# Kernel optimization log

Measured on AMD Instinct MI355X. Metric: run time of the kernel, lower is better.

The kernel has to match this reference:

```python
import jax, jax.numpy as jnp
import numpy as np

# BERT-base dims; 768 and max_sent_num=64 come from the module/config.
N, S, V, D, L, H, F = 8, 512, 30522, 768, 12, 12, 3072
DH = D // H
MAX_SENT = 64
LN_EPS = 1e-12
SCALE = float(np.sqrt(DH))


def _ln(x, g, b):
    m = jnp.mean(x, axis=-1, keepdims=True)
    v = jnp.mean(jnp.square(x - m), axis=-1, keepdims=True)
    return (x - m) * jax.lax.rsqrt(v + LN_EPS) * g + b


def setup_inputs() -> dict:
    key = jax.random.key(0)
    ks = jax.random.split(key, 10)
    # random token ids in a range avoiding the special ids 102/103
    ids = jax.random.randint(ks[0], (N, S), 999, 30000, dtype=jnp.int32)
    # variable per-doc sentence region -> ragged number of [MASK](103) separators (8..64)
    cutoff = jax.random.randint(ks[1], (N, 1), 64, S + 1)
    pos = jnp.arange(S)[None, :]
    sent_pos = ((pos % 8) == 7) & (pos < cutoff)
    ids = jnp.where(sent_pos, 103, ids)
    ids = ids.at[:, 0].set(102)  # exactly one [SEP]=102 per doc (required by the slice-assign)
    amask = jnp.ones((N, S), dtype=jnp.int32)
    g = lambda k, shape: 0.02 * jax.random.normal(k, shape, dtype=jnp.float32)
    inp = dict(input_ids_bert=ids, attention_mask_bert=amask)
    inp["tok_emb"] = g(ks[2], (V, D))
    inp["pos_emb"] = g(ks[3], (S, D))
    inp["emb_ln_g"] = jnp.ones((D,), jnp.float32)
    inp["emb_ln_b"] = jnp.zeros((D,), jnp.float32)
    inp["Wqkv"] = g(ks[4], (L, D, 3 * D))
    inp["bqkv"] = jnp.zeros((L, 3 * D), jnp.float32)
    inp["Wo"] = g(ks[5], (L, D, D))
    inp["bo"] = jnp.zeros((L, D), jnp.float32)
    inp["ln1_g"] = jnp.ones((L, D), jnp.float32)
    inp["ln1_b"] = jnp.zeros((L, D), jnp.float32)
    inp["W1"] = g(ks[6], (L, D, F))
    inp["b1"] = jnp.zeros((L, F), jnp.float32)
    inp["W2"] = g(ks[7], (L, F, D))
    inp["b2"] = jnp.zeros((L, D), jnp.float32)
    inp["ln2_g"] = jnp.ones((L, D), jnp.float32)
    inp["ln2_b"] = jnp.zeros((L, D), jnp.float32)
    return inp


def _bert(ids, amask, tok_emb, pos_emb, emb_ln_g, emb_ln_b,
          Wqkv, bqkv, Wo, bo, ln1_g, ln1_b, W1, b1, W2, b2, ln2_g, ln2_b):
    x = tok_emb[ids] + pos_emb[None, :, :]            # [N,S,D]
    x = _ln(x, emb_ln_g, emb_ln_b)
    bias = (1.0 - amask[:, None, None, :].astype(x.dtype)) * -1e9  # [N,1,1,S]

    def layer(x, p):
        wqkv, bq, wo, bo_, g1, b1n, w1, b1f, w2, b2f, g2, b2n = p
        qkv = x @ wqkv + bq
        q, k, v = jnp.split(qkv, 3, axis=-1)
        q = q.reshape(N, S, H, DH)
        k = k.reshape(N, S, H, DH)
        v = v.reshape(N, S, H, DH)
        att = jnp.einsum('bqhd,bkhd->bhqk', q, k) / SCALE + bias
        att = jax.nn.softmax(att, axis=-1)
        o = jnp.einsum('bhqk,bkhd->bqhd', att, v).reshape(N, S, D)
        x2 = _ln(x + o @ wo + bo_, g1, b1n)
        h = jax.nn.gelu(x2 @ w1 + b1f, approximate=False)
        return _ln(x2 + h @ w2 + b2f, g2, b2n), None

    x, _ = jax.lax.scan(layer, x, (Wqkv, bqkv, Wo, bo, ln1_g, ln1_b, W1, b1, W2, b2, ln2_g, ln2_b))
    return x


def _gather_scatter(ids, h):
    # Vectorized form of the per-doc python loop:
    #   out[doc, :n_sent] = concat([cls_emb(102), sent_embs(103)])[:-1]
    mask_sent = ids == 103
    mask_cls = ids == 102
    n_cls = mask_cls.sum(axis=1, keepdims=True)              # == 1 per doc
    total_sent = mask_sent.sum(axis=1, keepdims=True)        # ragged count
    rank_sent = jnp.cumsum(mask_sent, axis=1) - 1
    rank_cls = jnp.cumsum(mask_cls, axis=1) - 1
    dest = jnp.where(mask_cls, rank_cls,
                     jnp.where(mask_sent, n_cls + rank_sent, MAX_SENT))
    valid = (mask_cls | mask_sent) & (dest < total_sent) & (dest < MAX_SENT)
    dest_safe = jnp.where(valid, dest, MAX_SENT)             # dump invalid into scratch row
    vals = jnp.where(valid[..., None], h, 0.0)
    out = jnp.zeros((ids.shape[0], MAX_SENT + 1, D), dtype=h.dtype)
    out = out.at[jnp.arange(ids.shape[0])[:, None], dest_safe].set(vals)
    return out[:, :MAX_SENT]


def reference(input_ids_bert, attention_mask_bert, tok_emb, pos_emb, emb_ln_g, emb_ln_b,
              Wqkv, bqkv, Wo, bo, ln1_g, ln1_b, W1, b1, W2, b2, ln2_g, ln2_b):
    h = _bert(input_ids_bert, attention_mask_bert, tok_emb, pos_emb, emb_ln_g, emb_ln_b,
              Wqkv, bqkv, Wo, bo, ln1_g, ln1_b, W1, b1, W2, b2, ln2_g, ln2_b)
    return _gather_scatter(input_ids_bert, h)
```

## Files before the change

kernel.cpp:

```cpp
#include <hip/hip_runtime.h>
#include <hip/hip_bf16.h>

#define DEV static __device__ __forceinline__

using short8 = __attribute__((ext_vector_type(8))) short;
using f32x4 = __attribute__((ext_vector_type(4))) float;

DEV short f2bf(float f) {
  union { float f; unsigned u; } x; x.f = f;
  unsigned r = x.u + 0x7fffu + ((x.u >> 16) & 1u);
  return (short)(r >> 16);
}

DEV void gload16(const void* g, void* lds) {
  __builtin_amdgcn_global_load_lds(
      (const __attribute__((address_space(1))) void*)g,
      (__attribute__((address_space(3))) void*)lds, 16, 0, 0);
}

__global__ __launch_bounds__(256) void transpose_all_k(
    const float* __restrict__ Wqkv, const float* __restrict__ Wo,
    const float* __restrict__ W1, const float* __restrict__ W2,
    short* __restrict__ wqkvT, short* __restrict__ woT,
    short* __restrict__ w1T, short* __restrict__ w2T)
{
  __shared__ short t[64][72];
  const int b = blockIdx.x, tid = threadIdx.x;
  const float* in; short* out; int K, N, tt, nt;
  if (b < 432)       { in = Wqkv; out = wqkvT; K = 768;  N = 2304; tt = b;        nt = 36; }
  else if (b < 576)  { in = Wo;   out = woT;   K = 768;  N = 768;  tt = b - 432;  nt = 12; }
  else if (b < 1152) { in = W1;   out = w1T;   K = 768;  N = 3072; tt = b - 576;  nt = 48; }
  else               { in = W2;   out = w2T;   K = 3072; N = 768;  tt = b - 1152; nt = 12; }
  const int n0 = (tt % nt) * 64, k0 = (tt / nt) * 64;
  #pragma unroll
  for (int p = 0; p < 4; ++p) {
    int r = p * 16 + (tid >> 4), c4 = tid & 15;
    float4 v = *reinterpret_cast<const float4*>(in + (size_t)(k0 + r) * N + n0 + c4 * 4);
    t[r][c4 * 4 + 0] = f2bf(v.x);
    t[r][c4 * 4 + 1] = f2bf(v.y);
    t[r][c4 * 4 + 2] = f2bf(v.z);
    t[r][c4 * 4 + 3] = f2bf(v.w);
  }
  __syncthreads();
  #pragma unroll
  for (int q = 0; q < 2; ++q) {
    int n = tid >> 2, kc = (tid & 3) + q * 4;
    short8 o;
    #pragma unroll
    for (int j = 0; j < 8; ++j) o[j] = t[kc * 8 + j][n];
    *reinterpret_cast<short8*>(out + (size_t)(n0 + n) * K + k0 + kc * 8) = o;
  }
}

template <int BM, int EPI>
__global__ __launch_bounds__(256) void gemm_bt(
    const short* __restrict__ A, const short* __restrict__ Bt,
    const float* __restrict__ bias, const float* __restrict__ resid,
    void* __restrict__ Cout, int M, int Nn, int K)
{
  constexpr int AW = BM / 64;
  constexpr int MI = BM / 32;
  __shared__ short As[BM * 32];
  __shared__ short Bs[128 * 32];
  const int tid = threadIdx.x, lane = tid & 63, w = tid >> 6;
  const int wr = w >> 1, wc = w & 1;
  const int l15 = lane & 15, l4 = lane >> 4;
  const int m0 = blockIdx.y * BM, n0 = blockIdx.x * 128;
  const int crow = lane >> 2, ccol = (lane & 3) * 8;

  f32x4 acc[MI][4] = {};

  for (int k0 = 0; k0 < K; k0 += 32) {
    #pragma unroll
    for (int s = 0; s < AW; ++s) {
      int c = w * AW + s;
      gload16(A + (size_t)(m0 + c * 16 + crow) * K + k0 + ccol, &As[c * 512]);
    }
    #pragma unroll
    for (int s = 0; s < 2; ++s) {
      int c = w * 2 + s;
      gload16(Bt + (size_t)(n0 + c * 16 + crow) * K + k0 + ccol, &Bs[c * 512]);
    }
    __syncthreads();

    short8 af[MI], bfr[4];
    #pragma unroll
    for (int i = 0; i < MI; ++i)
      af[i] = *reinterpret_cast<const short8*>(&As[(wr * (BM / 2) + i * 16 + l15) * 32 + l4 * 8]);
    #pragma unroll
    for (int j = 0; j < 4; ++j)
      bfr[j] = *reinterpret_cast<const short8*>(&Bs[(wc * 64 + j * 16 + l15) * 32 + l4 * 8]);
    #pragma unroll
    for (int i = 0; i < MI; ++i)
      #pragma unroll
      for (int j = 0; j < 4; ++j)
        acc[i][j] = __builtin_amdgcn_mfma_f32_16x16x32_bf16(af[i], bfr[j], acc[i][j], 0, 0, 0);
    __syncthreads();
  }

  #pragma unroll
  for (int i = 0; i < MI; ++i) {
    #pragma unroll
    for (int j = 0; j < 4; ++j) {
      #pragma unroll
      for (int r = 0; r < 4; ++r) {
        int row = m0 + wr * (BM / 2) + i * 16 + l4 * 4 + r;
        int col = n0 + wc * 64 + j * 16 + l15;
        float v = acc[i][j][r] + bias[col];
        if constexpr (EPI == 1) v = 0.5f * v * (1.0f + erff(v * 0.70710678118654752f));
        ((short*)Cout)[(size_t)row * Nn + col] = f2bf(v);
      }
    }
  }
}

__global__ __launch_bounds__(256) void gemm_sk(
    const short* __restrict__ A, const short* __restrict__ Bt,
    float* __restrict__ p0, float* __restrict__ p1,
    int M, int Nn, int Kstride, int Klen)
{
  __shared__ short As[128 * 32];
  __shared__ short Bs[128 * 32];
  const int tid = threadIdx.x, lane = tid & 63, w = tid >> 6;
  const int wr = w >> 1, wc = w & 1;
  const int l15 = lane & 15, l4 = lane >> 4;
  const int m0 = blockIdx.y * 128, n0 = blockIdx.x * 128;
  const int koff = blockIdx.z * Klen;
  const int crow = lane >> 2, ccol = (lane & 3) * 8;

  f32x4 acc[4][4] = {};

  for (int k0 = 0; k0 < Klen; k0 += 32) {
    #pragma unroll
    for (int s = 0; s < 2; ++s) {
      int c = w * 2 + s;
      gload16(A + (size_t)(m0 + c * 16 + crow) * Kstride + koff + k0 + ccol, &As[c * 512]);
    }
    #pragma unroll
    for (int s = 0; s < 2; ++s) {
      int c = w * 2 + s;
      gload16(Bt + (size_t)(n0 + c * 16 + crow) * Kstride + koff + k0 + ccol, &Bs[c * 512]);
    }
    __syncthreads();

    short8 af[4], bfr[4];
    #pragma unroll
    for (int i = 0; i < 4; ++i)
      af[i] = *reinterpret_cast<const short8*>(&As[(wr * 64 + i * 16 + l15) * 32 + l4 * 8]);
    #pragma unroll
    for (int j = 0; j < 4; ++j)
      bfr[j] = *reinterpret_cast<const short8*>(&Bs[(wc * 64 + j * 16 + l15) * 32 + l4 * 8]);
    #pragma unroll
    for (int i = 0; i < 4; ++i)
      #pragma unroll
      for (int j = 0; j < 4; ++j)
        acc[i][j] = __builtin_amdgcn_mfma_f32_16x16x32_bf16(af[i], bfr[j], acc[i][j], 0, 0, 0);
    __syncthreads();
  }

  float* P = blockIdx.z ? p1 : p0;
  #pragma unroll
  for (int i = 0; i < 4; ++i)
    #pragma unroll
    for (int j = 0; j < 4; ++j)
      #pragma unroll
      for (int r = 0; r < 4; ++r) {
        int row = m0 + wr * 64 + i * 16 + l4 * 4 + r;
        int col = n0 + wc * 64 + j * 16 + l15;
        P[(size_t)row * Nn + col] = acc[i][j][r];
      }
}

__global__ __launch_bounds__(256) void attn_k(
    const short* __restrict__ qkv, const int* __restrict__ amask,
    short* __restrict__ out)
{
  __shared__ short Kl[64][72];
  __shared__ short Vt[64][68];
  __shared__ short Pl[4][16][72];
  const int b = blockIdx.z, h = blockIdx.y, qt = blockIdx.x;
  const int tid = threadIdx.x, lane = tid & 63, w = tid >> 6;
  const int l15 = lane & 15, l4 = lane >> 4;
  const int tok0 = b * 512;
  const int q0 = qt * 64 + w * 16;

  short8 qf[2];
  #pragma unroll
  for (int kk = 0; kk < 2; ++kk)
    qf[kk] = *reinterpret_cast<const short8*>(
        qkv + (size_t)(tok0 + q0 + l15) * 2304 + h * 64 + kk * 32 + l4 * 8);

  f32x4 oacc[4] = {};
  float mrow[4], lrow[4];
  #pragma unroll
  for (int r = 0; r < 4; ++r) { mrow[r] = -1e30f; lrow[r] = 0.f; }

  for (int kt0 = 0; kt0 < 512; kt0 += 64) {
    #pragma unroll
    for (int i = 0; i < 2; ++i) {
      int c = tid + i * 256;
      int r = c >> 3, dc = c & 7;
      short8 v = *reinterpret_cast<const short8*>(
          qkv + (size_t)(tok0 + kt0 + r) * 2304 + 768 + h * 64 + dc * 8);
      *reinterpret_cast<short8*>(&Kl[r][dc * 8]) = v;
    }
    #pragma unroll
    for (int i = 0; i < 2; ++i) {
      int c = tid + i * 256;
      int r = c >> 3, dc = c & 7;
      short8 v = *reinterpret_cast<const short8*>(
          qkv + (size_t)(tok0 + kt0 + r) * 2304 + 1536 + h * 64 + dc * 8);
      #pragma unroll
      for (int j = 0; j < 8; ++j) Vt[dc * 8 + j][r] = v[j];
    }
    __syncthreads();

    f32x4 sacc[4] = {};
    #pragma unroll
    for (int t = 0; t < 4; ++t) {
      #pragma unroll
      for (int kk = 0; kk < 2; ++kk) {
        short8 kf = *reinterpret_cast<const short8*>(&Kl[t * 16 + l15][kk * 32 + l4 * 8]);
        sacc[t] = __builtin_amdgcn_mfma_f32_16x16x32_bf16(qf[kk], kf, sacc[t], 0, 0, 0);
      }
    }
    float p[4][4];
    #pragma unroll
    for (int t = 0; t < 4; ++t) {
      int ktok = kt0 + t * 16 + l15;
      float biasv = amask[b * 512 + ktok] ? 0.f : -1e9f;
      #pragma unroll
      for (int r = 0; r < 4; ++r) p[t][r] = sacc[t][r] * 0.125f + biasv;
    }
    #pragma unroll
    for (int r = 0; r < 4; ++r) {
      float mx = fmaxf(fmaxf(p[0][r], p[1][r]), fmaxf(p[2][r], p[3][r]));
      #pragma unroll
      for (int s = 1; s <= 8; s <<= 1) mx = fmaxf(mx, __shfl_xor(mx, s, 64));
      float mnew = fmaxf(mrow[r], mx);
      float alpha = __expf(mrow[r] - mnew);
      mrow[r] = mnew;
      float sum = 0.f;
      #pragma unroll
      for (int t = 0; t < 4; ++t) { p[t][r] = __expf(p[t][r] - mnew); sum += p[t][r]; }
      #pragma unroll
      for (int s = 1; s <= 8; s <<= 1) sum += __shfl_xor(sum, s, 64);
      lrow[r] = lrow[r] * alpha + sum;
      #pragma unroll
      for (int t = 0; t < 4; ++t) oacc[t][r] *= alpha;
    }
    #pragma unroll
    for (int t = 0; t < 4; ++t)
      #pragma unroll
      for (int r = 0; r < 4; ++r)
        Pl[w][l4 * 4 + r][t * 16 + l15] = f2bf(p[t][r]);
    __syncthreads();
    #pragma unroll
    for (int kk = 0; kk < 2; ++kk) {
      short8 pf = *reinterpret_cast<const short8*>(&Pl[w][l15][kk * 32 + l4 * 8]);
      #pragma unroll
      for (int t = 0; t < 4; ++t) {
        const unsigned* vp = reinterpret_cast<const unsigned*>(&Vt[t * 16 + l15][0]);
        union { short8 s; unsigned u[4]; } vu;
        #pragma unroll
        for (int w2 = 0; w2 < 4; ++w2) vu.u[w2] = vp[kk * 16 + l4 * 4 + w2];
        oacc[t] = __builtin_amdgcn_mfma_f32_16x16x32_bf16(pf, vu.s, oacc[t], 0, 0, 0);
      }
    }
    __syncthreads();
  }

  #pragma unroll
  for (int t = 0; t < 4; ++t)
    #pragma unroll
    for (int r = 0; r < 4; ++r) {
      int tok = tok0 + q0 + l4 * 4 + r;
      int dh = t * 16 + l15;
      out[(size_t)tok * 768 + h * 64 + dh] = f2bf(oacc[t][r] / lrow[r]);
    }
}

__global__ __launch_bounds__(256) void ln2_k(
    const float* __restrict__ p0, const float* __restrict__ p1,
    const float* __restrict__ bias, const float* __restrict__ resid,
    const float* __restrict__ g, const float* __restrict__ be,
    float* __restrict__ xf, short* __restrict__ xb)
{
  const int t = blockIdx.x, tid = threadIdx.x;
  const size_t base = (size_t)t * 768;
  float v[3], s = 0.f, ss = 0.f;
  #pragma unroll
  for (int i = 0; i < 3; ++i) {
    int c = tid + i * 256;
    v[i] = p0[base + c] + p1[base + c] + bias[c] + resid[base + c];
    s += v[i]; ss += v[i] * v[i];
  }
  __shared__ float red[4][2];
  #pragma unroll
  for (int m = 1; m <= 32; m <<= 1) { s += __shfl_xor(s, m, 64); ss += __shfl_xor(ss, m, 64); }
  int w = tid >> 6;
  if ((tid & 63) == 0) { red[w][0] = s; red[w][1] = ss; }
  __syncthreads();
  s = red[0][0] + red[1][0] + red[2][0] + red[3][0];
  ss = red[0][1] + red[1][1] + red[2][1] + red[3][1];
  float mean = s * (1.f / 768.f);
  float var = ss * (1.f / 768.f) - mean * mean;
  float rs = rsqrtf(var + 1e-12f);
  #pragma unroll
  for (int i = 0; i < 3; ++i) {
    int c = tid + i * 256;
    float o = (v[i] - mean) * rs * g[c] + be[c];
    xf[base + c] = o;
    xb[base + c] = f2bf(o);
  }
}

__global__ __launch_bounds__(256) void embed_ln_k(
    const int* __restrict__ ids, const float* __restrict__ tok_emb,
    const float* __restrict__ pos_emb, const float* __restrict__ g,
    const float* __restrict__ be, float* __restrict__ xf, short* __restrict__ xb)
{
  const int t = blockIdx.x, tid = threadIdx.x;
  const int id = ids[t], sp = t & 511;
  float v[3], s = 0.f, ss = 0.f;
  #pragma unroll
  for (int i = 0; i < 3; ++i) {
    int c = tid + i * 256;
    v[i] = tok_emb[(size_t)id * 768 + c] + pos_emb[(size_t)sp * 768 + c];
    s += v[i]; ss += v[i] * v[i];
  }
  __shared__ float red[4][2];
  #pragma unroll
  for (int m = 1; m <= 32; m <<= 1) { s += __shfl_xor(s, m, 64); ss += __shfl_xor(ss, m, 64); }
  int w = tid >> 6;
  if ((tid & 63) == 0) { red[w][0] = s; red[w][1] = ss; }
  __syncthreads();
  s = red[0][0] + red[1][0] + red[2][0] + red[3][0];
  ss = red[0][1] + red[1][1] + red[2][1] + red[3][1];
  float mean = s * (1.f / 768.f);
  float var = ss * (1.f / 768.f) - mean * mean;
  float rs = rsqrtf(var + 1e-12f);
  #pragma unroll
  for (int i = 0; i < 3; ++i) {
    int c = tid + i * 256;
    float o = (v[i] - mean) * rs * g[c] + be[c];
    xf[(size_t)t * 768 + c] = o;
    xb[(size_t)t * 768 + c] = f2bf(o);
  }
}

__global__ __launch_bounds__(512) void gather_k(
    const int* __restrict__ ids, const float* __restrict__ x, float* __restrict__ out)
{
  const int doc = blockIdx.x, tid = threadIdx.x;
  const int lane = tid & 63, w = tid >> 6;
  __shared__ int src[64];
  __shared__ int wave_sent[8];
  __shared__ int cls_pos;
  if (tid < 64) src[tid] = -1;
  if (tid == 0) cls_pos = 0x7fffffff;
  __syncthreads();

  const int id = ids[doc * 512 + tid];
  const bool is_sent = (id == 103);
  const unsigned long long m = __ballot(is_sent);
  if (lane == 0) wave_sent[w] = __popcll(m);
  if (id == 102) atomicMin(&cls_pos, tid);
  __syncthreads();

  int total = 0, prefix = 0;
  #pragma unroll
  for (int i = 0; i < 8; ++i) {
    int c = wave_sent[i];
    if (i < w) prefix += c;
    total += c;
  }
  if (is_sent) {
    unsigned long long lt = lane ? (~0ULL >> (64 - lane)) : 0ULL;
    int d = 1 + prefix + __popcll(m & lt);
    if (d < total && d < 64) src[d] = tid;
  }
  if (tid == 0 && total > 0 && cls_pos != 0x7fffffff) src[0] = cls_pos;
  __syncthreads();

  for (int i = tid; i < 64 * 192; i += 512) {
    int row = i / 192, c4 = i - row * 192;
    int sp = src[row];
    float4 v = make_float4(0.f, 0.f, 0.f, 0.f);
    if (sp >= 0)
      v = reinterpret_cast<const float4*>(x + (size_t)(doc * 512 + sp) * 768)[c4];
    reinterpret_cast<float4*>(out + (size_t)doc * 64 * 768)[i] = v;
  }
}

extern "C" void kernel_launch(void* const* d_in, const int* in_sizes, int n_in,
                              void* d_out, int out_size, void* d_ws, size_t ws_size,
                              hipStream_t stream)
{
  const int* ids = (const int*)d_in[0];
  const int* am = (const int*)d_in[1];
  const float* tok_emb = (const float*)d_in[2];
  const float* pos_emb = (const float*)d_in[3];
  const float* eg = (const float*)d_in[4];
  const float* eb = (const float*)d_in[5];
  const float* Wqkv = (const float*)d_in[6];
  const float* bqkv = (const float*)d_in[7];
  const float* Wo = (const float*)d_in[8];
  const float* bo = (const float*)d_in[9];
  const float* g1 = (const float*)d_in[10];
  const float* b1n = (const float*)d_in[11];
  const float* W1 = (const float*)d_in[12];
  const float* b1f = (const float*)d_in[13];
  const float* W2 = (const float*)d_in[14];
  const float* b2f = (const float*)d_in[15];
  const float* g2 = (const float*)d_in[16];
  const float* b2n = (const float*)d_in[17];

  char* ws = (char*)d_ws;
  float* x_f   = (float*)(ws);
  short* x_b   = (short*)(ws + 12582912);
  float* x2_f  = (float*)(ws + 18874368);
  short* x2_b  = (short*)(ws + 31457280);
  float* y_f   = (float*)(ws + 37748736);
  short* qkv   = (short*)(ws + 50331648);
  float* skp1b = (float*)(ws + 50331648);
  short* attn  = (short*)(ws + 69206016);
  short* hb    = (short*)(ws + 75497472);
  float* skp1a = (float*)(ws + 75497472);
  short* wqkvT = (short*)(ws + 100663296);
  short* woT   = (short*)(ws + 104202240);
  short* w1T   = (short*)(ws + 105381888);
  short* w2T   = (short*)(ws + 110100480);

  embed_ln_k<<<4096, 256, 0, stream>>>(ids, tok_emb, pos_emb, eg, eb, x_f, x_b);

  for (int l = 0; l < 12; ++l) {
    transpose_all_k<<<1728, 256, 0, stream>>>(
        Wqkv + (size_t)l * 768 * 2304, Wo + (size_t)l * 768 * 768,
        W1 + (size_t)l * 768 * 3072, W2 + (size_t)l * 3072 * 768,
        wqkvT, woT, w1T, w2T);

    gemm_bt<128, 0><<<dim3(18, 32), 256, 0, stream>>>(
        x_b, wqkvT, bqkv + (size_t)l * 2304, nullptr, qkv, 4096, 2304, 768);
    attn_k<<<dim3(8, 12, 8), 256, 0, stream>>>(qkv, am, attn);

    gemm_sk<<<dim3(6, 32, 2), 256, 0, stream>>>(
        attn, woT, y_f, skp1a, 4096, 768, 768, 384);
    ln2_k<<<4096, 256, 0, stream>>>(
        y_f, skp1a, bo + (size_t)l * 768, x_f,
        g1 + (size_t)l * 768, b1n + (size_t)l * 768, x2_f, x2_b);

    gemm_bt<128, 1><<<dim3(24, 32), 256, 0, stream>>>(
        x2_b, w1T, b1f + (size_t)l * 3072, nullptr, hb, 4096, 3072, 768);

    gemm_sk<<<dim3(6, 32, 2), 256, 0, stream>>>(
        hb, w2T, y_f, skp1b, 4096, 768, 3072, 1536);
    ln2_k<<<4096, 256, 0, stream>>>(
        y_f, skp1b, b2f + (size_t)l * 768, x2_f,
        g2 + (size_t)l * 768, b2n + (size_t)l * 768, x_f, x_b);
  }

  gather_k<<<8, 512, 0, stream>>>(ids, x_f, (float*)d_out);
}
```

Measured before the change: 2.324 ms.

## Store split-K partials as bf16 and deepen GEMM K-step to 64

```diff
diff --git a/kernel.cpp b/kernel.cpp
--- a/kernel.cpp
+++ b/kernel.cpp
@@ -10,6 +10,11 @@
   union { float f; unsigned u; } x; x.f = f;
   unsigned r = x.u + 0x7fffu + ((x.u >> 16) & 1u);
   return (short)(r >> 16);
+}
+
+DEV float bf2f(short s) {
+  union { unsigned u; float f; } x; x.u = ((unsigned)(unsigned short)s) << 16;
+  return x.f;
 }
 
 DEV void gload16(const void* g, void* lds) {
@@ -60,8 +65,8 @@
 {
   constexpr int AW = BM / 64;
   constexpr int MI = BM / 32;
-  __shared__ short As[BM * 32];
-  __shared__ short Bs[128 * 32];
+  __shared__ short As[2 * BM * 32];
+  __shared__ short Bs[2 * 128 * 32];
   const int tid = threadIdx.x, lane = tid & 63, w = tid >> 6;
   const int wr = w >> 1, wc = w & 1;
   const int l15 = lane & 15, l4 = lane >> 4;
@@ -70,31 +75,41 @@
 
   f32x4 acc[MI][4] = {};
 
-  for (int k0 = 0; k0 < K; k0 += 32) {
-    #pragma unroll
-    for (int s = 0; s < AW; ++s) {
-      int c = w * AW + s;
-      gload16(A + (size_t)(m0 + c * 16 + crow) * K + k0 + ccol, &As[c * 512]);
-    }
-    #pragma unroll
-    for (int s = 0; s < 2; ++s) {
-      int c = w * 2 + s;
-      gload16(Bt + (size_t)(n0 + c * 16 + crow) * K + k0 + ccol, &Bs[c * 512]);
-    }
-    __syncthreads();
-
-    short8 af[MI], bfr[4];
-    #pragma unroll
-    for (int i = 0; i < MI; ++i)
-      af[i] = *reinterpret_cast<const short8*>(&As[(wr * (BM / 2) + i * 16 + l15) * 32 + l4 * 8]);
-    #pragma unroll
-    for (int j = 0; j < 4; ++j)
-      bfr[j] = *reinterpret_cast<const short8*>(&Bs[(wc * 64 + j * 16 + l15) * 32 + l4 * 8]);
-    #pragma unroll
-    for (int i = 0; i < MI; ++i)
+  for (int k0 = 0; k0 < K; k0 += 64) {
+    #pragma unroll
+    for (int ks = 0; ks < 2; ++ks) {
+      #pragma unroll
+      for (int s = 0; s < AW; ++s) {
+        int c = w * AW + s;
+        gload16(A + (size_t)(m0 + c * 16 + crow) * K + k0 + ks * 32 + ccol,
+                &As[ks * BM * 32 + c * 512]);
+      }
+      #pragma unroll
+      for (int s = 0; s < 2; ++s) {
+        int c = w * 2 + s;
+        gload16(Bt + (size_t)(n0 + c * 16 + crow) * K + k0 + ks * 32 + ccol,
+                &Bs[ks * 128 * 32 + c * 512]);
+      }
+    }
+    __syncthreads();
+
+    #pragma unroll
+    for (int ks = 0; ks < 2; ++ks) {
+      short8 af[MI], bfr[4];
+      #pragma unroll
+      for (int i = 0; i < MI; ++i)
+        af[i] = *reinterpret_cast<const short8*>(
+            &As[ks * BM * 32 + (wr * (BM / 2) + i * 16 + l15) * 32 + l4 * 8]);
       #pragma unroll
       for (int j = 0; j < 4; ++j)
-        acc[i][j] = __builtin_amdgcn_mfma_f32_16x16x32_bf16(af[i], bfr[j], acc[i][j], 0, 0, 0);
+        bfr[j] = *reinterpret_cast<const short8*>(
+            &Bs[ks * 128 * 32 + (wc * 64 + j * 16 + l15) * 32 + l4 * 8]);
+      #pragma unroll
+      for (int i = 0; i < MI; ++i)
+        #pragma unroll
+        for (int j = 0; j < 4; ++j)
+          acc[i][j] = __builtin_amdgcn_mfma_f32_16x16x32_bf16(af[i], bfr[j], acc[i][j], 0, 0, 0);
+    }
     __syncthreads();
   }
 
@@ -116,11 +131,11 @@
 
 __global__ __launch_bounds__(256) void gemm_sk(
     const short* __restrict__ A, const short* __restrict__ Bt,
-    float* __restrict__ p0, float* __restrict__ p1,
+    short* __restrict__ p0, short* __restrict__ p1,
     int M, int Nn, int Kstride, int Klen)
 {
-  __shared__ short As[128 * 32];
-  __shared__ short Bs[128 * 32];
+  __shared__ short As[2 * 128 * 32];
+  __shared__ short Bs[2 * 128 * 32];
   const int tid = threadIdx.x, lane = tid & 63, w = tid >> 6;
   const int wr = w >> 1, wc = w & 1;
   const int l15 = lane & 15, l4 = lane >> 4;
@@ -130,35 +145,45 @@
 
   f32x4 acc[4][4] = {};
 
-  for (int k0 = 0; k0 < Klen; k0 += 32) {
-    #pragma unroll
-    for (int s = 0; s < 2; ++s) {
-      int c = w * 2 + s;
-      gload16(A + (size_t)(m0 + c * 16 + crow) * Kstride + koff + k0 + ccol, &As[c * 512]);
-    }
-    #pragma unroll
-    for (int s = 0; s < 2; ++s) {
-      int c = w * 2 + s;
-      gload16(Bt + (size_t)(n0 + c * 16 + crow) * Kstride + koff + k0 + ccol, &Bs[c * 512]);
-    }
-    __syncthreads();
-
-    short8 af[4], bfr[4];
-    #pragma unroll
-    for (int i = 0; i < 4; ++i)
-      af[i] = *reinterpret_cast<const short8*>(&As[(wr * 64 + i * 16 + l15) * 32 + l4 * 8]);
-    #pragma unroll
-    for (int j = 0; j < 4; ++j)
-      bfr[j] = *reinterpret_cast<const short8*>(&Bs[(wc * 64 + j * 16 + l15) * 32 + l4 * 8]);
-    #pragma unroll
-    for (int i = 0; i < 4; ++i)
+  for (int k0 = 0; k0 < Klen; k0 += 64) {
+    #pragma unroll
+    for (int ks = 0; ks < 2; ++ks) {
+      #pragma unroll
+      for (int s = 0; s < 2; ++s) {
+        int c = w * 2 + s;
+        gload16(A + (size_t)(m0 + c * 16 + crow) * Kstride + koff + k0 + ks * 32 + ccol,
+                &As[ks * 4096 + c * 512]);
+      }
+      #pragma unroll
+      for (int s = 0; s < 2; ++s) {
+        int c = w * 2 + s;
+        gload16(Bt + (size_t)(n0 + c * 16 + crow) * Kstride + koff + k0 + ks * 32 + ccol,
+                &Bs[ks * 4096 + c * 512]);
+      }
+    }
+    __syncthreads();
+
+    #pragma unroll
+    for (int ks = 0; ks < 2; ++ks) {
+      short8 af[4], bfr[4];
+      #pragma unroll
+      for (int i = 0; i < 4; ++i)
+        af[i] = *reinterpret_cast<const short8*>(
+            &As[ks * 4096 + (wr * 64 + i * 16 + l15) * 32 + l4 * 8]);
       #pragma unroll
       for (int j = 0; j < 4; ++j)
-        acc[i][j] = __builtin_amdgcn_mfma_f32_16x16x32_bf16(af[i], bfr[j], acc[i][j], 0, 0, 0);
-    __syncthreads();
-  }
-
-  float* P = blockIdx.z ? p1 : p0;
+        bfr[j] = *reinterpret_cast<const short8*>(
+            &Bs[ks * 4096 + (wc * 64 + j * 16 + l15) * 32 + l4 * 8]);
+      #pragma unroll
+      for (int i = 0; i < 4; ++i)
+        #pragma unroll
+        for (int j = 0; j < 4; ++j)
+          acc[i][j] = __builtin_amdgcn_mfma_f32_16x16x32_bf16(af[i], bfr[j], acc[i][j], 0, 0, 0);
+    }
+    __syncthreads();
+  }
+
+  short* P = blockIdx.z ? p1 : p0;
   #pragma unroll
   for (int i = 0; i < 4; ++i)
     #pragma unroll
@@ -167,7 +192,7 @@
       for (int r = 0; r < 4; ++r) {
         int row = m0 + wr * 64 + i * 16 + l4 * 4 + r;
         int col = n0 + wc * 64 + j * 16 + l15;
-        P[(size_t)row * Nn + col] = acc[i][j][r];
+        P[(size_t)row * Nn + col] = f2bf(acc[i][j][r]);
       }
 }
 
@@ -281,7 +306,7 @@
 }
 
 __global__ __launch_bounds__(256) void ln2_k(
-    const float* __restrict__ p0, const float* __restrict__ p1,
+    const short* __restrict__ p0, const short* __restrict__ p1,
     const float* __restrict__ bias, const float* __restrict__ resid,
     const float* __restrict__ g, const float* __restrict__ be,
     float* __restrict__ xf, short* __restrict__ xb)
@@ -292,7 +317,7 @@
   #pragma unroll
   for (int i = 0; i < 3; ++i) {
     int c = tid + i * 256;
-    v[i] = p0[base + c] + p1[base + c] + bias[c] + resid[base + c];
+    v[i] = bf2f(p0[base + c]) + bf2f(p1[base + c]) + bias[c] + resid[base + c];
     s += v[i]; ss += v[i] * v[i];
   }
   __shared__ float red[4][2];
@@ -421,12 +446,12 @@
   short* x_b   = (short*)(ws + 12582912);
   float* x2_f  = (float*)(ws + 18874368);
   short* x2_b  = (short*)(ws + 31457280);
-  float* y_f   = (float*)(ws + 37748736);
+  short* skp0  = (short*)(ws + 37748736);
   short* qkv   = (short*)(ws + 50331648);
-  float* skp1b = (float*)(ws + 50331648);
+  short* skp1b = (short*)(ws + 50331648);
   short* attn  = (short*)(ws + 69206016);
   short* hb    = (short*)(ws + 75497472);
-  float* skp1a = (float*)(ws + 75497472);
+  short* skp1a = (short*)(ws + 75497472);
   short* wqkvT = (short*)(ws + 100663296);
   short* woT   = (short*)(ws + 104202240);
   short* w1T   = (short*)(ws + 105381888);
@@ -445,18 +470,18 @@
     attn_k<<<dim3(8, 12, 8), 256, 0, stream>>>(qkv, am, attn);
 
     gemm_sk<<<dim3(6, 32, 2), 256, 0, stream>>>(
-        attn, woT, y_f, skp1a, 4096, 768, 768, 384);
+        attn, woT, skp0, skp1a, 4096, 768, 768, 384);
     ln2_k<<<4096, 256, 0, stream>>>(
-        y_f, skp1a, bo + (size_t)l * 768, x_f,
+        skp0, skp1a, bo + (size_t)l * 768, x_f,
         g1 + (size_t)l * 768, b1n + (size_t)l * 768, x2_f, x2_b);
 
     gemm_bt<128, 1><<<dim3(24, 32), 256, 0, stream>>>(
         x2_b, w1T, b1f + (size_t)l * 3072, nullptr, hb, 4096, 3072, 768);
 
     gemm_sk<<<dim3(6, 32, 2), 256, 0, stream>>>(
-        hb, w2T, y_f, skp1b, 4096, 768, 3072, 1536);
+        hb, w2T, skp0, skp1b, 4096, 768, 3072, 1536);
     ln2_k<<<4096, 256, 0, stream>>>(
-        y_f, skp1b, b2f + (size_t)l * 768, x2_f,
+        skp0, skp1b, b2f + (size_t)l * 768, x2_f,
         g2 + (size_t)l * 768, b2n + (size_t)l * 768, x_f, x_b);
   }
 
```

New measurement: 2.211 ms. -4.8%, faster.
